# Kernel optimization log

Hardware: AMD Instinct MI355X
Metric: run time of the kernel (lower is better)

The kernel has to match this reference:

```python
import jax, jax.numpy as jnp
import numpy as np

N, IN_RAW, H, E, UNROLLS = 1024, 10, 96, 16384, 2

def _p(key, shape):
    return jax.random.normal(key, shape, dtype=jnp.float32) * 0.05

def setup_inputs() -> dict:
    key = jax.random.key(0)
    ks = jax.random.split(key, 24)
    x = jax.random.normal(ks[0], (N, IN_RAW), dtype=jnp.float32)
    edge_index = jax.random.randint(ks[1], (2, E), 0, N, dtype=jnp.int64)
    adj = jax.random.randint(ks[2], (N, N), 0, 2, dtype=jnp.int32)
    return {
        'x': x, 'edge_index': edge_index, 'adj': adj,
        # init_layer
        'W_init': _p(ks[3], (H, IN_RAW - 1)), 'b_init': _p(ks[4], (H,)),
        # GatedGraphConv (num_layers=1): weight [H,H], GRUCell params
        'W_ggc': _p(ks[5], (H, H)),
        'W_ih': _p(ks[6], (3 * H, H)), 'W_hh': _p(ks[7], (3 * H, H)),
        'b_ih': _p(ks[8], (3 * H,)), 'b_hh': _p(ks[9], (3 * H,)),
        # edge_attention: Linear(2H->H), Linear(H->1)
        'Wa1': _p(ks[10], (H, 2 * H)), 'ba1': _p(ks[11], (H,)),
        'Wa2': _p(ks[12], (1, H)), 'ba2': _p(ks[13], (1,)),
        # out MLP
        'Wo1': _p(ks[14], (H, H)), 'bo1': _p(ks[15], (H,)),
        'Wo2': _p(ks[16], (H, H)), 'bo2': _p(ks[17], (H,)),
        # heads
        'Wp1': _p(ks[18], (1, H)), 'bp1': _p(ks[19], (1,)),
        'Wp2': _p(ks[20], (1, H)), 'bp2': _p(ks[21], (1,)),
    }

def _leaky(v):
    return jnp.where(v >= 0, v, 0.01 * v)  # LeakyReLU default slope

def _ggnn_forward(x, edge_index, adj,
                  W_init, b_init, W_ggc, W_ih, W_hh, b_ih, b_hh,
                  Wa1, ba1, Wa2, ba2, Wo1, bo1, Wo2, bo2,
                  Wp1, bp1, Wp2, bp2):
    src, tgt = edge_index[0], edge_index[1]
    x = x[:, :-1]                                   # data.x[:, :-1]
    x = _leaky(x @ W_init.T + b_init)               # [N,H]
    adj_mask = (adj == 1)
    for _ in range(UNROLLS):
        # GatedGraphConv, 1 layer, aggr='mean'
        m = x @ W_ggc                               # [N,H]
        s = jax.ops.segment_sum(m[src], tgt, num_segments=N)
        cnt = jax.ops.segment_sum(jnp.ones((E,), x.dtype), tgt, num_segments=N)
        agg = s / jnp.maximum(cnt, 1.0)[:, None]    # mean, 0 for isolated nodes
        # GRUCell(agg, x)
        gi = agg @ W_ih.T + b_ih
        gh = x @ W_hh.T + b_hh
        ir, iz, inn = jnp.split(gi, 3, axis=1)
        hr, hz, hn = jnp.split(gh, 3, axis=1)
        r = jax.nn.sigmoid(ir + hr)
        z = jax.nn.sigmoid(iz + hz)
        n = jnp.tanh(inn + r * hn)
        x = (1.0 - z) * n + z * x
        # edge attention: concat(x_i, x_j) -> Linear(2H->H) decomposed into
        # two [H,H] halves so the NxNx2H concat tensor is never materialized.
        hi = x @ Wa1[:, :H].T                       # acts on t1 (row i)
        hj = x @ Wa1[:, H:].T                       # acts on t2 (row j)
        h = jax.nn.sigmoid(hi[:, None, :] + hj[None, :, :] + ba1)  # [N,N,H]
        coeffs = jax.nn.sigmoid(h @ Wa2[0] + ba2[0])               # [N,N]
        coeffs = jnp.where(adj_mask, coeffs, 0.0)
        x = coeffs @ x
    x = _leaky(x @ Wo1.T + bo1)
    x = _leaky(x @ Wo2.T + bo2)
    out1 = jax.nn.sigmoid(x @ Wp1.T + bp1)
    out2 = jax.nn.sigmoid(x @ Wp2.T + bp2)
    return out1, out2

def reference(x, edge_index, adj,
              W_init, b_init, W_ggc, W_ih, W_hh, b_ih, b_hh,
              Wa1, ba1, Wa2, ba2, Wo1, bo1, Wo2, bo2,
              Wp1, bp1, Wp2, bp2):
    return _ggnn_forward(x, edge_index, adj,
                         W_init, b_init, W_ggc, W_ih, W_hh, b_ih, b_hh,
                         Wa1, ba1, Wa2, ba2, Wo1, bo1, Wo2, bo2,
                         Wp1, bp1, Wp2, bp2)
```

## Files before the change

### kernel.cpp

```cpp
#include <hip/hip_runtime.h>

#define Nn 1024
#define Hh 96
#define Ee 16384
#define IN_K 9
#define IN_STRIDE 10
#define NH (Nn * Hh)
#define XS 128
#define SLOTS 64

__device__ __forceinline__ float sigf(float v) {
    return __builtin_amdgcn_rcpf(1.0f + __expf(-v));
}
__device__ __forceinline__ float tanhfast(float v) {
    float e = __expf(2.0f * v);
    return (e - 1.0f) * __builtin_amdgcn_rcpf(e + 1.0f);
}
__device__ __forceinline__ float leakyf(float v) {
    return v >= 0.0f ? v : 0.01f * v;
}

__global__ __launch_bounds__(256) void setup_kernel(
    const float* __restrict__ W_hh, const float* __restrict__ Wa1,
    const float* __restrict__ Wo1, const float* __restrict__ Wo2,
    const float* __restrict__ W_ggc, const float* __restrict__ W_ih,
    const float* __restrict__ x_in, const float* __restrict__ W_init,
    const float* __restrict__ b_init,
    float* __restrict__ Wt_hh, float* __restrict__ Wt_a1i,
    float* __restrict__ Wt_a1j, float* __restrict__ Wt_o1,
    float* __restrict__ Wt_o2, float* __restrict__ Wf,
    int* __restrict__ deg, float* __restrict__ xA)
{
    int gt = blockIdx.x * 256 + threadIdx.x;
    if (gt < Nn) deg[gt] = 0;
    if (gt < 64512) {
        int idx = gt;
        if (idx < 27648) {
            int k = idx / 288, c = idx % 288;
            Wt_hh[idx] = W_hh[c * 96 + k];
        } else if ((idx -= 27648) < 9216) {
            int k = idx / 96, h = idx % 96;
            Wt_a1i[idx] = Wa1[h * 192 + k];
        } else if ((idx -= 9216) < 9216) {
            int k = idx / 96, h = idx % 96;
            Wt_a1j[idx] = Wa1[h * 192 + 96 + k];
        } else if ((idx -= 9216) < 9216) {
            int k = idx / 96, j = idx % 96;
            Wt_o1[idx] = Wo1[j * 96 + k];
        } else {
            idx -= 9216;
            int k = idx / 96, j = idx % 96;
            Wt_o2[idx] = Wo2[j * 96 + k];
        }
    }
    if (gt < 27648) {
        int k = gt / 288, c = gt % 288;
        const float* g = W_ggc + k * 96;
        const float* w = W_ih + c * 96;
        float acc = 0.0f;
        for (int j = 0; j < 96; ++j) acc += g[j] * w[j];
        Wf[gt] = acc;
    }
    if (gt < NH) {
        int n = gt / Hh, j = gt - n * Hh;
        const float* xr = x_in + n * IN_STRIDE;
        const float* wr = W_init + j * IN_K;
        float acc = b_init[j];
#pragma unroll
        for (int k = 0; k < IN_K; ++k) acc += xr[k] * wr[k];
        xA[n * XS + j] = leakyf(acc);
    }
}

__global__ __launch_bounds__(256) void edges_kernel(
    const int* __restrict__ ei, int* __restrict__ deg, int* __restrict__ bucket)
{
    int e = blockIdx.x * 256 + threadIdx.x;
    if (e >= Ee) return;
    int src = ei[e];
    int tgt = ei[Ee + e];
    int slot = atomicAdd(&deg[tgt], 1);
    if (slot < SLOTS) bucket[tgt * SLOTS + slot] = src;
}

__global__ __launch_bounds__(384) void gru_kernel(
    const float* __restrict__ xA, const int* __restrict__ deg,
    const int* __restrict__ bucket,
    const float* __restrict__ Wf, const float* __restrict__ Wt_hh,
    const float* __restrict__ b_ih, const float* __restrict__ b_hh,
    const float* __restrict__ Wt_a1i, const float* __restrict__ Wt_a1j,
    const float* __restrict__ ba1,
    float* __restrict__ xB, float* __restrict__ Ei, float* __restrict__ EjT,
    float* __restrict__ xZero)
{
    __shared__ float Pp[2][2][Hh];
    __shared__ float Pm[2][Hh];
    __shared__ float Xr[2][Hh];
    __shared__ float Xo[2][Hh];
    __shared__ float red6[2][2][Hh][6];
    __shared__ float redp[2][2][Hh][2];
    int tid = threadIdx.x;
    int half = tid / 192;
    int loc = tid - half * 192;
    int r = loc / Hh, h = loc - r * Hh;
    int n = blockIdx.x * 2 + r;
    {
        int d = deg[n];
        int dc = d < SLOTS ? d : SLOTS;
        const int* bk = bucket + n * SLOTS;
        float acc = 0.0f;
        for (int s = half; s < dc; s += 2)
            acc += xA[bk[s] * XS + h];
        Pp[half][r][h] = acc;
        if (half == 0) Xr[r][h] = xA[n * XS + h];
        else           xZero[n * XS + h] = 0.0f;
    }
    __syncthreads();
    if (half == 0) {
        float inv = __builtin_amdgcn_rcpf(fmaxf((float)deg[n], 1.0f));
        Pm[r][h] = (Pp[0][r][h] + Pp[1][r][h]) * inv;
    }
    __syncthreads();
    {
        const float* Pr = Pm[r];
        const float* xr = Xr[r];
        const float* pf = Wf + h;
        const float* ph = Wt_hh + h;
        float gir = 0.f, giz = 0.f, gin = 0.f;
        float ghr = 0.f, ghz = 0.f, ghn = 0.f;
        int k0 = half * 48;
#pragma unroll 4
        for (int k = k0; k < k0 + 48; ++k) {
            float a = Pr[k];
            float xv = xr[k];
            int o = k * 288;
            gir += a * pf[o];
            giz += a * pf[o + 96];
            gin += a * pf[o + 192];
            ghr += xv * ph[o];
            ghz += xv * ph[o + 96];
            ghn += xv * ph[o + 192];
        }
        red6[half][r][h][0] = gir;
        red6[half][r][h][1] = giz;
        red6[half][r][h][2] = gin;
        red6[half][r][h][3] = ghr;
        red6[half][r][h][4] = ghz;
        red6[half][r][h][5] = ghn;
    }
    __syncthreads();
    if (half == 0) {
        float gir = b_ih[h] + red6[0][r][h][0] + red6[1][r][h][0];
        float giz = b_ih[Hh + h] + red6[0][r][h][1] + red6[1][r][h][1];
        float gin = b_ih[2 * Hh + h] + red6[0][r][h][2] + red6[1][r][h][2];
        float ghr = b_hh[h] + red6[0][r][h][3] + red6[1][r][h][3];
        float ghz = b_hh[Hh + h] + red6[0][r][h][4] + red6[1][r][h][4];
        float ghn = b_hh[2 * Hh + h] + red6[0][r][h][5] + red6[1][r][h][5];
        float rr = sigf(gir + ghr);
        float z = sigf(giz + ghz);
        float nn2 = tanhfast(gin + rr * ghn);
        float xo = (1.0f - z) * nn2 + z * Xr[r][h];
        xB[n * XS + h] = xo;
        Xo[r][h] = xo;
    }
    __syncthreads();
    {
        const float* row = Xo[r];
        const float* wi = Wt_a1i + h;
        const float* wj = Wt_a1j + h;
        float a = 0.0f, bb = 0.0f;
        int k0 = half * 48;
#pragma unroll 4
        for (int k = k0; k < k0 + 48; ++k) {
            float xv = row[k];
            a += xv * wi[k * 96];
            bb += xv * wj[k * 96];
        }
        redp[half][r][h][0] = a;
        redp[half][r][h][1] = bb;
    }
    __syncthreads();
    if (half == 0) {
        float a = redp[0][r][h][0] + redp[1][r][h][0];
        float bb = redp[0][r][h][1] + redp[1][r][h][1];
        Ei[n * Hh + h] = __expf(-(a + ba1[h]));
        EjT[h * Nn + n] = __expf(-bb);
    }
}

__global__ __launch_bounds__(512) void attn_kernel(
    const float* __restrict__ Ei, const float* __restrict__ EjT,
    const float* __restrict__ Wa2, const float* __restrict__ ba2,
    const int* __restrict__ adj, const float* __restrict__ xB,
    float* __restrict__ xOut)
{
    __shared__ __align__(16) float wa2[Hh];
    __shared__ __align__(16) float eis[4][Hh];
    __shared__ __align__(16) float C[4][512];
    __shared__ float red[4][4][Hh];
    int tid = threadIdx.x;
    int ig = blockIdx.x >> 1;
    int jh = blockIdx.x & 1;
    int i0 = ig * 4;
    int jbase = jh * 512;
    if (tid < Hh) wa2[tid] = Wa2[tid];
    if (tid < 4 * Hh) {
        int r = tid / Hh, h = tid - r * Hh;
        eis[r][h] = Ei[(i0 + r) * Hh + h];
    }
    __syncthreads();
    {
        int j = jbase + tid;
        int m0 = adj[(i0 + 0) * Nn + j];
        int m1 = adj[(i0 + 1) * Nn + j];
        int m2 = adj[(i0 + 2) * Nn + j];
        int m3 = adj[(i0 + 3) * Nn + j];
        float s0 = 0.f, s1 = 0.f, s2 = 0.f, s3 = 0.f;
#pragma unroll 4
        for (int k = 0; k < Hh; ++k) {
            float e = EjT[k * Nn + j];
            float wk = wa2[k];
            s0 += __builtin_amdgcn_rcpf(fmaf(eis[0][k], e, 1.0f)) * wk;
            s1 += __builtin_amdgcn_rcpf(fmaf(eis[1][k], e, 1.0f)) * wk;
            s2 += __builtin_amdgcn_rcpf(fmaf(eis[2][k], e, 1.0f)) * wk;
            s3 += __builtin_amdgcn_rcpf(fmaf(eis[3][k], e, 1.0f)) * wk;
        }
        float b2 = ba2[0];
        C[0][tid] = (m0 == 1) ? sigf(s0 + b2) : 0.0f;
        C[1][tid] = (m1 == 1) ? sigf(s1 + b2) : 0.0f;
        C[2][tid] = (m2 == 1) ? sigf(s2 + b2) : 0.0f;
        C[3][tid] = (m3 == 1) ? sigf(s3 + b2) : 0.0f;
    }
    __syncthreads();
    {
        int q = tid >> 7;
        int h = tid & 127;
        if (h < Hh) {
            int jq = q * 128;
            const float* xc = xB + (jbase + jq) * XS + h;
            const float* c0 = &C[0][jq];
            const float* c1 = &C[1][jq];
            const float* c2 = &C[2][jq];
            const float* c3 = &C[3][jq];
            float a0 = 0.f, a1 = 0.f, a2 = 0.f, a3 = 0.f;
#pragma unroll 4
            for (int j = 0; j < 128; ++j) {
                float xv = xc[j * XS];
                a0 += c0[j] * xv;
                a1 += c1[j] * xv;
                a2 += c2[j] * xv;
                a3 += c3[j] * xv;
            }
            red[q][0][h] = a0;
            red[q][1][h] = a1;
            red[q][2][h] = a2;
            red[q][3][h] = a3;
        }
        __syncthreads();
        if (h < Hh) {
            float v = red[0][q][h] + red[1][q][h] + red[2][q][h] + red[3][q][h];
            atomicAdd(&xOut[(i0 + q) * XS + h], v);
        }
    }
}

__global__ __launch_bounds__(384) void head_kernel(
    const float* __restrict__ xA,
    const float* __restrict__ Wt_o1, const float* __restrict__ bo1,
    const float* __restrict__ Wt_o2, const float* __restrict__ bo2,
    const float* __restrict__ Wp1, const float* __restrict__ bp1,
    const float* __restrict__ Wp2, const float* __restrict__ bp2,
    float* __restrict__ out)
{
    __shared__ float xr[4][Hh];
    __shared__ float t1[4][Hh];
    __shared__ float t2[4][Hh];
    int tid = threadIdx.x;
    int r = tid / Hh, h = tid - r * Hh;
    int n = blockIdx.x * 4 + r;
    xr[r][h] = xA[n * XS + h];
    __syncthreads();
    {
        const float* w = Wt_o1 + h;
        float acc = bo1[h];
        for (int k = 0; k < Hh; ++k) acc += xr[r][k] * w[k * 96];
        t1[r][h] = leakyf(acc);
    }
    __syncthreads();
    {
        const float* w = Wt_o2 + h;
        float acc = bo2[h];
        for (int k = 0; k < Hh; ++k) acc += t1[r][k] * w[k * 96];
        t2[r][h] = leakyf(acc);
    }
    __syncthreads();
    if (h == 0) {
        float s1 = 0.f;
        for (int k = 0; k < Hh; ++k) s1 += t2[r][k] * Wp1[k];
        out[n] = sigf(s1 + bp1[0]);
    } else if (h == 1) {
        float s2 = 0.f;
        for (int k = 0; k < Hh; ++k) s2 += t2[r][k] * Wp2[k];
        out[Nn + n] = sigf(s2 + bp2[0]);
    }
}

extern "C" void kernel_launch(void* const* d_in, const int* in_sizes, int n_in,
                              void* d_out, int out_size, void* d_ws, size_t ws_size,
                              hipStream_t stream)
{
    const float* x_in   = (const float*)d_in[0];
    const int*   ei     = (const int*)d_in[1];
    const int*   adj    = (const int*)d_in[2];
    const float* W_init = (const float*)d_in[3];
    const float* b_init = (const float*)d_in[4];
    const float* W_ggc  = (const float*)d_in[5];
    const float* W_ih   = (const float*)d_in[6];
    const float* W_hh   = (const float*)d_in[7];
    const float* b_ih   = (const float*)d_in[8];
    const float* b_hh   = (const float*)d_in[9];
    const float* Wa1    = (const float*)d_in[10];
    const float* ba1    = (const float*)d_in[11];
    const float* Wa2    = (const float*)d_in[12];
    const float* ba2    = (const float*)d_in[13];
    const float* Wo1    = (const float*)d_in[14];
    const float* bo1    = (const float*)d_in[15];
    const float* Wo2    = (const float*)d_in[16];
    const float* bo2    = (const float*)d_in[17];
    const float* Wp1    = (const float*)d_in[18];
    const float* bp1    = (const float*)d_in[19];
    const float* Wp2    = (const float*)d_in[20];
    const float* bp2    = (const float*)d_in[21];
    float* out = (float*)d_out;

    float* ws     = (float*)d_ws;
    float* xA     = ws;
    float* xB     = xA + Nn * XS;
    float* xC     = xB + Nn * XS;
    float* Ei     = xC + Nn * XS;
    float* EjT    = Ei + NH;
    float* Wt_hh  = EjT + NH;
    float* Wf     = Wt_hh + 27648;
    float* Wt_a1i = Wf + 27648;
    float* Wt_a1j = Wt_a1i + 9216;
    float* Wt_o1  = Wt_a1j + 9216;
    float* Wt_o2  = Wt_o1 + 9216;
    int*   deg    = (int*)(Wt_o2 + 9216);
    int*   bucket = deg + Nn;

    setup_kernel<<<(NH + 255) / 256, 256, 0, stream>>>(
        W_hh, Wa1, Wo1, Wo2, W_ggc, W_ih, x_in, W_init, b_init,
        Wt_hh, Wt_a1i, Wt_a1j, Wt_o1, Wt_o2, Wf, deg, xA);
    edges_kernel<<<(Ee + 255) / 256, 256, 0, stream>>>(ei, deg, bucket);

    gru_kernel<<<Nn / 2, 384, 0, stream>>>(
        xA, deg, bucket, Wf, Wt_hh, b_ih, b_hh, Wt_a1i, Wt_a1j, ba1,
        xB, Ei, EjT, xC);
    attn_kernel<<<Nn / 2, 512, 0, stream>>>(
        Ei, EjT, Wa2, ba2, adj, xB, xC);
    gru_kernel<<<Nn / 2, 384, 0, stream>>>(
        xC, deg, bucket, Wf, Wt_hh, b_ih, b_hh, Wt_a1i, Wt_a1j, ba1,
        xB, Ei, EjT, xA);
    attn_kernel<<<Nn / 2, 512, 0, stream>>>(
        Ei, EjT, Wa2, ba2, adj, xB, xA);

    head_kernel<<<Nn / 4, 384, 0, stream>>>(
        xA, Wt_o1, bo1, Wt_o2, bo2, Wp1, bp1, Wp2, bp2, out);
}
```

Measured before the change: 197.3 us.

## Give each attention block a full row set, drop atomics, fuse output head

The attention kernel now covers all 1024 columns for a group of four rows in one 1024-thread block, replacing the two-block split. It reduces partial sums in shared memory and writes the result directly, so the output atomics and the zeroing of the output buffer in the GRU kernel both go away. The second-unroll attention kernel also computes the MLP head and both sigmoid outputs, which removes a separate launch. The trade-off is half as many blocks, each with 1024 threads and more shared memory, which may lower occupancy and parallelism on the device.

```diff
diff --git a/kernel.cpp b/kernel.cpp
--- a/kernel.cpp
+++ b/kernel.cpp
@@ -90,8 +90,7 @@
     const float* __restrict__ b_ih, const float* __restrict__ b_hh,
     const float* __restrict__ Wt_a1i, const float* __restrict__ Wt_a1j,
     const float* __restrict__ ba1,
-    float* __restrict__ xB, float* __restrict__ Ei, float* __restrict__ EjT,
-    float* __restrict__ xZero)
+    float* __restrict__ xB, float* __restrict__ Ei, float* __restrict__ EjT)
 {
     __shared__ float Pp[2][2][Hh];
     __shared__ float Pm[2][Hh];
@@ -109,11 +108,11 @@
         int dc = d < SLOTS ? d : SLOTS;
         const int* bk = bucket + n * SLOTS;
         float acc = 0.0f;
+#pragma unroll 4
         for (int s = half; s < dc; s += 2)
             acc += xA[bk[s] * XS + h];
         Pp[half][r][h] = acc;
         if (half == 0) Xr[r][h] = xA[n * XS + h];
-        else           xZero[n * XS + h] = 0.0f;
     }
     __syncthreads();
     if (half == 0) {
@@ -188,60 +187,56 @@
     }
 }
 
-__global__ __launch_bounds__(512) void attn_kernel(
+__global__ __launch_bounds__(1024) void attn_kernel_u0(
     const float* __restrict__ Ei, const float* __restrict__ EjT,
     const float* __restrict__ Wa2, const float* __restrict__ ba2,
     const int* __restrict__ adj, const float* __restrict__ xB,
     float* __restrict__ xOut)
 {
-    __shared__ __align__(16) float wa2[Hh];
-    __shared__ __align__(16) float eis[4][Hh];
-    __shared__ __align__(16) float C[4][512];
-    __shared__ float red[4][4][Hh];
+    __shared__ float sm[7648];
     int tid = threadIdx.x;
-    int ig = blockIdx.x >> 1;
-    int jh = blockIdx.x & 1;
-    int i0 = ig * 4;
-    int jbase = jh * 512;
-    if (tid < Hh) wa2[tid] = Wa2[tid];
-    if (tid < 4 * Hh) {
-        int r = tid / Hh, h = tid - r * Hh;
-        eis[r][h] = Ei[(i0 + r) * Hh + h];
-    }
-    __syncthreads();
-    {
-        int j = jbase + tid;
+    int i0 = blockIdx.x * 4;
+    if (tid < Hh) sm[tid] = Wa2[tid];
+    if (tid >= 128 && tid < 128 + 4 * Hh) {
+        int t = tid - 128;
+        int r = t / Hh, h = t - r * Hh;
+        sm[96 + t] = Ei[(i0 + r) * Hh + h];
+    }
+    __syncthreads();
+    {
+        int j = tid;
         int m0 = adj[(i0 + 0) * Nn + j];
         int m1 = adj[(i0 + 1) * Nn + j];
         int m2 = adj[(i0 + 2) * Nn + j];
         int m3 = adj[(i0 + 3) * Nn + j];
+        const float* e0 = sm + 96;
         float s0 = 0.f, s1 = 0.f, s2 = 0.f, s3 = 0.f;
 #pragma unroll 4
         for (int k = 0; k < Hh; ++k) {
             float e = EjT[k * Nn + j];
-            float wk = wa2[k];
-            s0 += __builtin_amdgcn_rcpf(fmaf(eis[0][k], e, 1.0f)) * wk;
-            s1 += __builtin_amdgcn_rcpf(fmaf(eis[1][k], e, 1.0f)) * wk;
-            s2 += __builtin_amdgcn_rcpf(fmaf(eis[2][k], e, 1.0f)) * wk;
-            s3 += __builtin_amdgcn_rcpf(fmaf(eis[3][k], e, 1.0f)) * wk;
+            float wk = sm[k];
+            s0 += __builtin_amdgcn_rcpf(fmaf(e0[k], e, 1.0f)) * wk;
+            s1 += __builtin_amdgcn_rcpf(fmaf(e0[96 + k], e, 1.0f)) * wk;
+            s2 += __builtin_amdgcn_rcpf(fmaf(e0[192 + k], e, 1.0f)) * wk;
+            s3 += __builtin_amdgcn_rcpf(fmaf(e0[288 + k], e, 1.0f)) * wk;
         }
         float b2 = ba2[0];
-        C[0][tid] = (m0 == 1) ? sigf(s0 + b2) : 0.0f;
-        C[1][tid] = (m1 == 1) ? sigf(s1 + b2) : 0.0f;
-        C[2][tid] = (m2 == 1) ? sigf(s2 + b2) : 0.0f;
-        C[3][tid] = (m3 == 1) ? sigf(s3 + b2) : 0.0f;
+        sm[480 + 0 * Nn + j] = (m0 == 1) ? sigf(s0 + b2) : 0.0f;
+        sm[480 + 1 * Nn + j] = (m1 == 1) ? sigf(s1 + b2) : 0.0f;
+        sm[480 + 2 * Nn + j] = (m2 == 1) ? sigf(s2 + b2) : 0.0f;
+        sm[480 + 3 * Nn + j] = (m3 == 1) ? sigf(s3 + b2) : 0.0f;
     }
     __syncthreads();
     {
         int q = tid >> 7;
         int h = tid & 127;
         if (h < Hh) {
-            int jq = q * 128;
-            const float* xc = xB + (jbase + jq) * XS + h;
-            const float* c0 = &C[0][jq];
-            const float* c1 = &C[1][jq];
-            const float* c2 = &C[2][jq];
-            const float* c3 = &C[3][jq];
+            int jb = q * 128;
+            const float* xc = xB + jb * XS + h;
+            const float* c0 = sm + 480 + 0 * Nn + jb;
+            const float* c1 = sm + 480 + 1 * Nn + jb;
+            const float* c2 = sm + 480 + 2 * Nn + jb;
+            const float* c3 = sm + 480 + 3 * Nn + jb;
             float a0 = 0.f, a1 = 0.f, a2 = 0.f, a3 = 0.f;
 #pragma unroll 4
             for (int j = 0; j < 128; ++j) {
@@ -251,57 +246,128 @@
                 a2 += c2[j] * xv;
                 a3 += c3[j] * xv;
             }
-            red[q][0][h] = a0;
-            red[q][1][h] = a1;
-            red[q][2][h] = a2;
-            red[q][3][h] = a3;
-        }
-        __syncthreads();
-        if (h < Hh) {
-            float v = red[0][q][h] + red[1][q][h] + red[2][q][h] + red[3][q][h];
-            atomicAdd(&xOut[(i0 + q) * XS + h], v);
-        }
-    }
-}
-
-__global__ __launch_bounds__(384) void head_kernel(
-    const float* __restrict__ xA,
+            sm[4576 + ((q * 4 + 0) * Hh) + h] = a0;
+            sm[4576 + ((q * 4 + 1) * Hh) + h] = a1;
+            sm[4576 + ((q * 4 + 2) * Hh) + h] = a2;
+            sm[4576 + ((q * 4 + 3) * Hh) + h] = a3;
+        }
+    }
+    __syncthreads();
+    if (tid < 4 * Hh) {
+        int r = tid / Hh, h = tid - r * Hh;
+        float v = 0.f;
+#pragma unroll
+        for (int q = 0; q < 8; ++q)
+            v += sm[4576 + ((q * 4 + r) * Hh) + h];
+        xOut[(i0 + r) * XS + h] = v;
+    }
+}
+
+__global__ __launch_bounds__(1024) void attn_kernel_u1(
+    const float* __restrict__ Ei, const float* __restrict__ EjT,
+    const float* __restrict__ Wa2, const float* __restrict__ ba2,
+    const int* __restrict__ adj, const float* __restrict__ xB,
     const float* __restrict__ Wt_o1, const float* __restrict__ bo1,
     const float* __restrict__ Wt_o2, const float* __restrict__ bo2,
     const float* __restrict__ Wp1, const float* __restrict__ bp1,
     const float* __restrict__ Wp2, const float* __restrict__ bp2,
     float* __restrict__ out)
 {
-    __shared__ float xr[4][Hh];
-    __shared__ float t1[4][Hh];
-    __shared__ float t2[4][Hh];
+    __shared__ float sm[7648];
     int tid = threadIdx.x;
-    int r = tid / Hh, h = tid - r * Hh;
-    int n = blockIdx.x * 4 + r;
-    xr[r][h] = xA[n * XS + h];
-    __syncthreads();
-    {
+    int i0 = blockIdx.x * 4;
+    if (tid < Hh) sm[tid] = Wa2[tid];
+    if (tid >= 128 && tid < 128 + 4 * Hh) {
+        int t = tid - 128;
+        int r = t / Hh, h = t - r * Hh;
+        sm[96 + t] = Ei[(i0 + r) * Hh + h];
+    }
+    __syncthreads();
+    {
+        int j = tid;
+        int m0 = adj[(i0 + 0) * Nn + j];
+        int m1 = adj[(i0 + 1) * Nn + j];
+        int m2 = adj[(i0 + 2) * Nn + j];
+        int m3 = adj[(i0 + 3) * Nn + j];
+        const float* e0 = sm + 96;
+        float s0 = 0.f, s1 = 0.f, s2 = 0.f, s3 = 0.f;
+#pragma unroll 4
+        for (int k = 0; k < Hh; ++k) {
+            float e = EjT[k * Nn + j];
+            float wk = sm[k];
+            s0 += __builtin_amdgcn_rcpf(fmaf(e0[k], e, 1.0f)) * wk;
+            s1 += __builtin_amdgcn_rcpf(fmaf(e0[96 + k], e, 1.0f)) * wk;
+            s2 += __builtin_amdgcn_rcpf(fmaf(e0[192 + k], e, 1.0f)) * wk;
+            s3 += __builtin_amdgcn_rcpf(fmaf(e0[288 + k], e, 1.0f)) * wk;
+        }
+        float b2 = ba2[0];
+        sm[480 + 0 * Nn + j] = (m0 == 1) ? sigf(s0 + b2) : 0.0f;
+        sm[480 + 1 * Nn + j] = (m1 == 1) ? sigf(s1 + b2) : 0.0f;
+        sm[480 + 2 * Nn + j] = (m2 == 1) ? sigf(s2 + b2) : 0.0f;
+        sm[480 + 3 * Nn + j] = (m3 == 1) ? sigf(s3 + b2) : 0.0f;
+    }
+    __syncthreads();
+    {
+        int q = tid >> 7;
+        int h = tid & 127;
+        if (h < Hh) {
+            int jb = q * 128;
+            const float* xc = xB + jb * XS + h;
+            const float* c0 = sm + 480 + 0 * Nn + jb;
+            const float* c1 = sm + 480 + 1 * Nn + jb;
+            const float* c2 = sm + 480 + 2 * Nn + jb;
+            const float* c3 = sm + 480 + 3 * Nn + jb;
+            float a0 = 0.f, a1 = 0.f, a2 = 0.f, a3 = 0.f;
+#pragma unroll 4
+            for (int j = 0; j < 128; ++j) {
+                float xv = xc[j * XS];
+                a0 += c0[j] * xv;
+                a1 += c1[j] * xv;
+                a2 += c2[j] * xv;
+                a3 += c3[j] * xv;
+            }
+            sm[4576 + ((q * 4 + 0) * Hh) + h] = a0;
+            sm[4576 + ((q * 4 + 1) * Hh) + h] = a1;
+            sm[4576 + ((q * 4 + 2) * Hh) + h] = a2;
+            sm[4576 + ((q * 4 + 3) * Hh) + h] = a3;
+        }
+    }
+    __syncthreads();
+    if (tid < 4 * Hh) {
+        int r = tid / Hh, h = tid - r * Hh;
+        float v = 0.f;
+#pragma unroll
+        for (int q = 0; q < 8; ++q)
+            v += sm[4576 + ((q * 4 + r) * Hh) + h];
+        sm[480 + r * Hh + h] = v;
+    }
+    __syncthreads();
+    if (tid < 4 * Hh) {
+        int r = tid / Hh, h = tid - r * Hh;
         const float* w = Wt_o1 + h;
+        const float* xr = sm + 480 + r * Hh;
         float acc = bo1[h];
-        for (int k = 0; k < Hh; ++k) acc += xr[r][k] * w[k * 96];
-        t1[r][h] = leakyf(acc);
-    }
-    __syncthreads();
-    {
+        for (int k = 0; k < Hh; ++k) acc += xr[k] * w[k * 96];
+        sm[864 + r * Hh + h] = leakyf(acc);
+    }
+    __syncthreads();
+    if (tid < 4 * Hh) {
+        int r = tid / Hh, h = tid - r * Hh;
         const float* w = Wt_o2 + h;
+        const float* xr = sm + 864 + r * Hh;
         float acc = bo2[h];
-        for (int k = 0; k < Hh; ++k) acc += t1[r][k] * w[k * 96];
-        t2[r][h] = leakyf(acc);
-    }
-    __syncthreads();
-    if (h == 0) {
-        float s1 = 0.f;
-        for (int k = 0; k < Hh; ++k) s1 += t2[r][k] * Wp1[k];
-        out[n] = sigf(s1 + bp1[0]);
-    } else if (h == 1) {
-        float s2 = 0.f;
-        for (int k = 0; k < Hh; ++k) s2 += t2[r][k] * Wp2[k];
-        out[Nn + n] = sigf(s2 + bp2[0]);
+        for (int k = 0; k < Hh; ++k) acc += xr[k] * w[k * 96];
+        sm[1248 + r * Hh + h] = leakyf(acc);
+    }
+    __syncthreads();
+    if (tid < 8) {
+        int r = tid >> 1, which = tid & 1;
+        const float* wp = which ? Wp2 : Wp1;
+        const float* xr = sm + 1248 + r * Hh;
+        float acc = 0.f;
+        for (int k = 0; k < Hh; ++k) acc += xr[k] * wp[k];
+        float b = which ? bp2[0] : bp1[0];
+        out[which * Nn + i0 + r] = sigf(acc + b);
     }
 }
 
@@ -355,15 +421,13 @@
 
     gru_kernel<<<Nn / 2, 384, 0, stream>>>(
         xA, deg, bucket, Wf, Wt_hh, b_ih, b_hh, Wt_a1i, Wt_a1j, ba1,
-        xB, Ei, EjT, xC);
-    attn_kernel<<<Nn / 2, 512, 0, stream>>>(
+        xB, Ei, EjT);
+    attn_kernel_u0<<<Nn / 4, 1024, 0, stream>>>(
         Ei, EjT, Wa2, ba2, adj, xB, xC);
     gru_kernel<<<Nn / 2, 384, 0, stream>>>(
         xC, deg, bucket, Wf, Wt_hh, b_ih, b_hh, Wt_a1i, Wt_a1j, ba1,
-        xB, Ei, EjT, xA);
-    attn_kernel<<<Nn / 2, 512, 0, stream>>>(
-        Ei, EjT, Wa2, ba2, adj, xB, xA);
-
-    head_kernel<<<Nn / 4, 384, 0, stream>>>(
-        xA, Wt_o1, bo1, Wt_o2, bo2, Wp1, bp1, Wp2, bp2, out);
-}
+        xB, Ei, EjT);
+    attn_kernel_u1<<<Nn / 4, 1024, 0, stream>>>(
+        Ei, EjT, Wa2, ba2, adj, xB,
+        Wt_o1, bo1, Wt_o2, bo2, Wp1, bp1, Wp2, bp2, out);
+}
```

After: 197.1 us. No clear change (-0.1%).
